# Kernel tuning notes

Hardware: AMD Instinct MI355X
Metric: run time of the kernel (lower is better)

Reference implementation:

```python
import jax, jax.numpy as jnp
import numpy as np

D_MODEL = 1024
N_HEADS = 16
D_HEAD = 64
GROUP_SIZE = 2
N_GROUPS = N_HEADS // GROUP_SIZE


def setup_inputs() -> dict:
    key = jax.random.key(0)
    k1, k2, k3, k4, k5 = jax.random.split(key, 5)
    def xavier(k, shape):
        fan_in, fan_out = shape[0], int(np.prod(shape[1:]))
        bound = float(np.sqrt(6.0 / (fan_in + fan_out)))
        return jax.random.uniform(k, shape, jnp.float32, -bound, bound)
    return {
        'resid': jax.random.normal(k1, (2, 2048, D_MODEL), jnp.float32),
        'W_Q': xavier(k2, (D_MODEL, N_HEADS, D_HEAD)),
        'W_K': xavier(k3, (D_MODEL, N_GROUPS, D_HEAD)),
        'W_V': xavier(k4, (D_MODEL, N_GROUPS, D_HEAD)),
        'W_out': xavier(k5, (D_HEAD, N_HEADS, D_MODEL)),
        'b_out': jnp.zeros((D_MODEL,), jnp.float32),
    }


def reference(resid, W_Q, W_K, W_V, W_out, b_out):
    batch, seq, _ = resid.shape
    # q: [b, s, n_heads, d_head] -> [b, s, n_groups, group_size, d_head]
    q = jnp.einsum('bsd,dhe->bshe', resid, W_Q)
    q = q.reshape(batch, seq, N_GROUPS, GROUP_SIZE, D_HEAD)
    k = jnp.einsum('bsd,dge->bsge', resid, W_K)  # [b, s, g, e]
    v = jnp.einsum('bsd,dge->bsge', resid, W_V)
    # scores: [b, g, group_size, qseq, kseq]
    scores = jnp.einsum('bqgre,bkge->bgrqk', q, k) / jnp.sqrt(jnp.float32(D_HEAD))
    causal_mask = jnp.triu(jnp.ones((seq, seq), bool), k=1)
    scores = jnp.where(causal_mask, jnp.float32(-1000000.0), scores)
    probs = jax.nn.softmax(scores, axis=-1)
    # z: [b, q, g, r, e]
    z = jnp.einsum('bgrqk,bkge->bqgre', probs, v)
    z = z.reshape(batch, seq, N_HEADS, D_HEAD)
    out = jnp.einsum('bshe,ehd->bsd', z, W_out) + b_out
    return out
```

## Files before the change

### kernel.cpp

```cpp
#include <hip/hip_runtime.h>

#define BATCH   2
#define SEQ     2048
#define DMODEL  1024
#define NHEADS  16
#define DHEAD   64
#define NGROUPS 8
#define NTOK    (BATCH * SEQ)
#define QKV_N   2048

typedef unsigned short ushort_t;
typedef unsigned int u32;
typedef __attribute__((ext_vector_type(8))) short short8;
typedef __attribute__((ext_vector_type(4))) float f32x4;

#define MFMA16(a, b, c) __builtin_amdgcn_mfma_f32_16x16x32_bf16((a), (b), (c), 0, 0, 0)

#define GLOAD16(gp, lp)                                                        \
    __builtin_amdgcn_global_load_lds(                                          \
        (const u32 __attribute__((address_space(1)))*)(gp),                    \
        (u32 __attribute__((address_space(3)))*)(lp), 16, 0, 0)

__device__ __forceinline__ ushort_t f2bu(float x) {
    unsigned u = __builtin_bit_cast(unsigned, x);
    unsigned r = (u + 0x7fffu + ((u >> 16) & 1u)) >> 16;
    return (ushort_t)r;
}

__global__ __launch_bounds__(256) void cvt_resid(
    const float* __restrict__ in, ushort_t* __restrict__ out)
{
    const int i4 = blockIdx.x * 256 + threadIdx.x;
    union { float4 v; float f[4]; } a;
    a.v = *reinterpret_cast<const float4*>(in + (size_t)i4 * 4);
    union { uint2 v; ushort_t u[4]; } o;
    #pragma unroll
    for (int j = 0; j < 4; ++j) o.u[j] = f2bu(a.f[j]);
    *reinterpret_cast<uint2*>(out + (size_t)i4 * 4) = o.v;
}

__global__ __launch_bounds__(256) void tr_wqkv(
    const float* __restrict__ Wq, const float* __restrict__ Wk,
    const float* __restrict__ Wv, ushort_t* __restrict__ Wt)
{
    __shared__ float Ws[64][65];
    const int t  = threadIdx.x;
    const int k0 = blockIdx.x * 64;
    const int n0 = blockIdx.y * 64;

    const float* src; int stride, boff;
    if (n0 < 1024)       { src = Wq; stride = 1024; boff = n0; }
    else if (n0 < 1536)  { src = Wk; stride = 512;  boff = n0 - 1024; }
    else                 { src = Wv; stride = 512;  boff = n0 - 1536; }

    #pragma unroll
    for (int i = 0; i < 4; ++i) {
        const int c = i * 256 + t;
        const int row = c >> 4, cc = (c & 15) * 4;
        union { float4 v; float f[4]; } a;
        a.v = *reinterpret_cast<const float4*>(src + (size_t)(k0 + row) * stride + boff + cc);
        #pragma unroll
        for (int j = 0; j < 4; ++j) Ws[row][cc + j] = a.f[j];
    }
    __syncthreads();
    #pragma unroll
    for (int i = 0; i < 2; ++i) {
        const int c = i * 256 + t;
        const int nr = c >> 3, kc = (c & 7) * 8;
        union { uint4 v; ushort_t u[8]; } o;
        #pragma unroll
        for (int j = 0; j < 8; ++j) o.u[j] = f2bu(Ws[kc + j][nr]);
        *reinterpret_cast<uint4*>(Wt + (size_t)(n0 + nr) * 1024 + k0 + kc) = o.v;
    }
}

__global__ __launch_bounds__(256) void tr_wout(
    const float* __restrict__ Wout, ushort_t* __restrict__ Wt)
{
    __shared__ float Ws[64][65];
    const int t  = threadIdx.x;
    const int d0 = blockIdx.x * 64;
    const int h  = blockIdx.y;

    #pragma unroll
    for (int i = 0; i < 4; ++i) {
        const int c = i * 256 + t;
        const int e = c >> 4, dd = (c & 15) * 4;
        union { float4 v; float f[4]; } a;
        a.v = *reinterpret_cast<const float4*>(Wout + (size_t)(e * 16 + h) * 1024 + d0 + dd);
        #pragma unroll
        for (int j = 0; j < 4; ++j) Ws[e][dd + j] = a.f[j];
    }
    __syncthreads();
    #pragma unroll
    for (int i = 0; i < 2; ++i) {
        const int c = i * 256 + t;
        const int dr = c >> 3, ec = (c & 7) * 8;
        union { uint4 v; ushort_t u[8]; } o;
        #pragma unroll
        for (int j = 0; j < 8; ++j) o.u[j] = f2bu(Ws[ec + j][dr]);
        *reinterpret_cast<uint4*>(Wt + (size_t)(d0 + dr) * 1024 + h * 64 + ec) = o.v;
    }
}

__global__ __launch_bounds__(256) void tr_v(
    const ushort_t* __restrict__ qkv, ushort_t* __restrict__ Vt)
{
    __shared__ ushort_t T[64][72];
    const int t  = threadIdx.x;
    const int s0 = blockIdx.x * 64;
    const int g  = blockIdx.y;
    const int b  = blockIdx.z;

    #pragma unroll
    for (int i = 0; i < 2; ++i) {
        const int c = i * 256 + t;
        const int row = c >> 3, ec = (c & 7) * 8;
        *reinterpret_cast<uint4*>(&T[row][ec]) =
            *reinterpret_cast<const uint4*>(
                qkv + (size_t)(b * SEQ + s0 + row) * QKV_N + 1536 + g * 64 + ec);
    }
    __syncthreads();
    #pragma unroll
    for (int i = 0; i < 2; ++i) {
        const int c = i * 256 + t;
        const int er = c >> 3, sc = (c & 7) * 8;
        union { uint4 v; ushort_t u[8]; } o;
        #pragma unroll
        for (int j = 0; j < 8; ++j) o.u[j] = T[sc + j][er];
        *reinterpret_cast<uint4*>(
            Vt + (size_t)((b * NGROUPS + g) * 64 + er) * SEQ + s0 + sc) = o.v;
    }
}

__global__ __launch_bounds__(256) void qkv_gemm(
    const ushort_t* __restrict__ A, const ushort_t* __restrict__ Bt,
    ushort_t* __restrict__ C)
{
    __shared__ ushort_t As[128][32];
    __shared__ ushort_t Bs[128][32];

    const int t = threadIdx.x;
    const int wave = t >> 6, lane = t & 63;
    const int quad = lane >> 4, x = lane & 15;
    const int wm = (wave >> 1) * 64, wn = (wave & 1) * 64;
    const int m0 = blockIdx.y * 128, n0 = blockIdx.x * 128;

    const int sr = lane >> 2;
    const int gc = (lane & 3) ^ (sr & 3);

    f32x4 acc[4][4];
    #pragma unroll
    for (int i = 0; i < 4; ++i)
        #pragma unroll
        for (int j = 0; j < 4; ++j) acc[i][j] = (f32x4)(0.f);

    const int swz = (quad ^ (x & 3)) * 8;

    for (int k0 = 0; k0 < 1024; k0 += 32) {
        #pragma unroll
        for (int s = 0; s < 2; ++s) {
            const int r0 = (wave * 2 + s) * 16;
            GLOAD16(A  + (size_t)(m0 + r0 + sr) * 1024 + k0 + gc * 8, &As[r0][0]);
            GLOAD16(Bt + (size_t)(n0 + r0 + sr) * 1024 + k0 + gc * 8, &Bs[r0][0]);
        }
        __syncthreads();
        short8 af[4], bf[4];
        #pragma unroll
        for (int mt = 0; mt < 4; ++mt)
            af[mt] = *reinterpret_cast<const short8*>(&As[wm + mt * 16 + x][swz]);
        #pragma unroll
        for (int nt = 0; nt < 4; ++nt)
            bf[nt] = *reinterpret_cast<const short8*>(&Bs[wn + nt * 16 + x][swz]);
        #pragma unroll
        for (int mt = 0; mt < 4; ++mt)
            #pragma unroll
            for (int nt = 0; nt < 4; ++nt)
                acc[mt][nt] = MFMA16(af[mt], bf[nt], acc[mt][nt]);
        __syncthreads();
    }

    #pragma unroll
    for (int mt = 0; mt < 4; ++mt)
        #pragma unroll
        for (int nt = 0; nt < 4; ++nt)
            #pragma unroll
            for (int r = 0; r < 4; ++r) {
                const int row = m0 + wm + mt * 16 + quad * 4 + r;
                const int col = n0 + wn + nt * 16 + x;
                C[(size_t)row * QKV_N + col] = f2bu(acc[mt][nt][r]);
            }
}

__global__ __launch_bounds__(256) void out_gemm(
    const ushort_t* __restrict__ A, const ushort_t* __restrict__ Bt,
    const float* __restrict__ bias, float* __restrict__ C)
{
    __shared__ ushort_t As[128][32];
    __shared__ ushort_t Bs[64][32];

    const int t = threadIdx.x;
    const int wave = t >> 6, lane = t & 63;
    const int quad = lane >> 4, x = lane & 15;
    const int wm = (wave >> 1) * 64, wn = (wave & 1) * 32;
    const int m0 = blockIdx.y * 128, n0 = blockIdx.x * 64;

    const int sr = lane >> 2;
    const int gc = (lane & 3) ^ (sr & 3);

    f32x4 acc[4][2];
    #pragma unroll
    for (int i = 0; i < 4; ++i)
        #pragma unroll
        for (int j = 0; j < 2; ++j) acc[i][j] = (f32x4)(0.f);

    const int swz = (quad ^ (x & 3)) * 8;

    for (int k0 = 0; k0 < 1024; k0 += 32) {
        #pragma unroll
        for (int s = 0; s < 2; ++s) {
            const int r0 = (wave * 2 + s) * 16;
            GLOAD16(A + (size_t)(m0 + r0 + sr) * 1024 + k0 + gc * 8, &As[r0][0]);
        }
        {
            const int r0 = wave * 16;
            GLOAD16(Bt + (size_t)(n0 + r0 + sr) * 1024 + k0 + gc * 8, &Bs[r0][0]);
        }
        __syncthreads();
        short8 af[4], bf[2];
        #pragma unroll
        for (int mt = 0; mt < 4; ++mt)
            af[mt] = *reinterpret_cast<const short8*>(&As[wm + mt * 16 + x][swz]);
        #pragma unroll
        for (int nt = 0; nt < 2; ++nt)
            bf[nt] = *reinterpret_cast<const short8*>(&Bs[wn + nt * 16 + x][swz]);
        #pragma unroll
        for (int mt = 0; mt < 4; ++mt)
            #pragma unroll
            for (int nt = 0; nt < 2; ++nt)
                acc[mt][nt] = MFMA16(af[mt], bf[nt], acc[mt][nt]);
        __syncthreads();
    }

    float bv[2];
    #pragma unroll
    for (int nt = 0; nt < 2; ++nt) bv[nt] = bias[n0 + wn + nt * 16 + x];

    #pragma unroll
    for (int mt = 0; mt < 4; ++mt)
        #pragma unroll
        for (int nt = 0; nt < 2; ++nt)
            #pragma unroll
            for (int r = 0; r < 4; ++r) {
                const int row = m0 + wm + mt * 16 + quad * 4 + r;
                const int col = n0 + wn + nt * 16 + x;
                C[(size_t)row * 1024 + col] = acc[mt][nt][r] + bv[nt];
            }
}

__global__ __launch_bounds__(512, 4) void attn(
    const ushort_t* __restrict__ qkv, const ushort_t* __restrict__ Vt,
    ushort_t* __restrict__ z)
{
    __shared__ ushort_t smem[3 * 64 * 72];
    ushort_t (*Ks)[72]  = (ushort_t(*)[72])(smem);
    ushort_t (*Vts)[72] = (ushort_t(*)[72])(smem + 64 * 72);
    ushort_t (*Ps)[72]  = (ushort_t(*)[72])(smem + 2 * 64 * 72);
    float* Ob = (float*)smem;
    float* Lb = (float*)(smem + 2 * 64 * 72);

    const int t = threadIdx.x;
    const int wave = t >> 6, lane = t & 63;
    const int quad = lane >> 4, x = lane & 15;
    const int rw = wave & 3;
    const int kw = wave >> 2;

    const int h  = blockIdx.x;
    const int qp = blockIdx.y;
    const int b  = blockIdx.z;
    const int g  = h >> 1;

    const int srow = t >> 3;
    const int sec  = (t & 7) * 8;

    const ushort_t* kbase = qkv + (size_t)(b * SEQ) * QKV_N + 1024 + g * DHEAD + sec;
    const ushort_t* vbase = Vt + (size_t)((b * NGROUPS + g) * 64 + srow) * SEQ + sec;

    #pragma unroll
    for (int phase = 0; phase < 2; ++phase) {
        const int qt = phase ? (31 - qp) : qp;
        const int qrow0 = qt * 64;

        short8 aq[2];
        {
            const size_t qr = (size_t)(b * SEQ + qrow0 + rw * 16 + x);
            #pragma unroll
            for (int ks = 0; ks < 2; ++ks)
                aq[ks] = *reinterpret_cast<const short8*>(
                    qkv + qr * QKV_N + h * DHEAD + ks * 32 + quad * 8);
        }

        f32x4 o[4];
        #pragma unroll
        for (int nt = 0; nt < 4; ++nt) o[nt] = (f32x4)(0.f);
        float l_acc[4] = {0.f, 0.f, 0.f, 0.f};

        uint4 kr, vr;
        kr = *reinterpret_cast<const uint4*>(kbase + (size_t)srow * QKV_N);
        vr = *reinterpret_cast<const uint4*>(vbase);

        for (int kt = 0; kt <= qt; ++kt) {
            __syncthreads();
            *reinterpret_cast<uint4*>(&Ks[srow][sec])  = kr;
            *reinterpret_cast<uint4*>(&Vts[srow][sec]) = vr;
            __syncthreads();

            if (kt < qt) {
                kr = *reinterpret_cast<const uint4*>(
                    kbase + (size_t)((kt + 1) * 64 + srow) * QKV_N);
                vr = *reinterpret_cast<const uint4*>(vbase + (kt + 1) * 64);
            }

            const bool diag  = (kt == qt);
            const bool wlive = !diag || (kw * 32 <= rw * 16 + 15);

            if (wlive) {
                f32x4 s[2];
                __builtin_amdgcn_s_setprio(1);
                #pragma unroll
                for (int nt = 0; nt < 2; ++nt) {
                    const bool live = !diag || (kw * 32 + nt * 16 <= rw * 16 + 15);
                    if (live) {
                        s[nt] = (f32x4)(0.f);
                        #pragma unroll
                        for (int ks = 0; ks < 2; ++ks) {
                            short8 bk = *reinterpret_cast<const short8*>(
                                &Ks[kw * 32 + nt * 16 + x][ks * 32 + quad * 8]);
                            s[nt] = MFMA16(aq[ks], bk, s[nt]);
                        }
                    }
                }
                __builtin_amdgcn_s_setprio(0);

                #pragma unroll
                for (int r = 0; r < 4; ++r) {
                    #pragma unroll
                    for (int nt = 0; nt < 2; ++nt) {
                        const bool live = !diag || (kw * 32 + nt * 16 <= rw * 16 + 15);
                        float p = 0.f;
                        if (live) {
                            const bool masked = diag &&
                                (kw * 32 + nt * 16 + x > rw * 16 + quad * 4 + r);
                            p = masked ? 0.f : __expf(s[nt][r] * 0.125f);
                        }
                        l_acc[r] += p;
                        Ps[rw * 16 + quad * 4 + r][kw * 32 + nt * 16 + x] = f2bu(p);
                    }
                }

                __builtin_amdgcn_s_setprio(1);
                {
                    short8 ap = *reinterpret_cast<const short8*>(
                        &Ps[rw * 16 + x][kw * 32 + quad * 8]);
                    #pragma unroll
                    for (int nt = 0; nt < 4; ++nt) {
                        short8 bv = *reinterpret_cast<const short8*>(
                            &Vts[nt * 16 + x][kw * 32 + quad * 8]);
                        o[nt] = MFMA16(ap, bv, o[nt]);
                    }
                }
                __builtin_amdgcn_s_setprio(0);
            }
        }

        __syncthreads();
        if (kw == 1) {
            #pragma unroll
            for (int nt = 0; nt < 4; ++nt)
                #pragma unroll
                for (int r = 0; r < 4; ++r)
                    Ob[(rw * 16 + quad * 4 + r) * 64 + nt * 16 + x] = o[nt][r];
            #pragma unroll
            for (int r = 0; r < 4; ++r)
                Lb[(rw * 16 + quad * 4 + r) * 16 + x] = l_acc[r];
        }
        __syncthreads();
        if (kw == 0) {
            #pragma unroll
            for (int nt = 0; nt < 4; ++nt)
                #pragma unroll
                for (int r = 0; r < 4; ++r)
                    o[nt][r] += Ob[(rw * 16 + quad * 4 + r) * 64 + nt * 16 + x];
            float inv[4];
            #pragma unroll
            for (int r = 0; r < 4; ++r) {
                float lr = l_acc[r] + Lb[(rw * 16 + quad * 4 + r) * 16 + x];
                #pragma unroll
                for (int off = 1; off < 16; off <<= 1)
                    lr += __shfl_xor(lr, off);
                inv[r] = 1.f / lr;
            }
            #pragma unroll
            for (int nt = 0; nt < 4; ++nt)
                #pragma unroll
                for (int r = 0; r < 4; ++r) {
                    const int row = qrow0 + rw * 16 + quad * 4 + r;
                    z[(size_t)(b * SEQ + row) * 1024 + h * DHEAD + nt * 16 + x] =
                        f2bu(o[nt][r] * inv[r]);
                }
        }
    }
}

extern "C" void kernel_launch(void* const* d_in, const int* in_sizes, int n_in,
                              void* d_out, int out_size, void* d_ws, size_t ws_size,
                              hipStream_t stream)
{
    const float* resid = (const float*)d_in[0];
    const float* Wq    = (const float*)d_in[1];
    const float* Wk    = (const float*)d_in[2];
    const float* Wv    = (const float*)d_in[3];
    const float* Wout  = (const float*)d_in[4];
    const float* bout  = (const float*)d_in[5];
    float* out = (float*)d_out;

    ushort_t* rbf   = (ushort_t*)d_ws;
    ushort_t* wqkvt = rbf   + (size_t)NTOK * DMODEL;
    ushort_t* woutt = wqkvt + (size_t)QKV_N * DMODEL;
    ushort_t* qkv   = woutt + (size_t)DMODEL * DMODEL;
    ushort_t* z     = qkv   + (size_t)NTOK * QKV_N;
    ushort_t* vt    = rbf;

    cvt_resid<<<dim3(NTOK * DMODEL / 1024), 256, 0, stream>>>(resid, rbf);
    tr_wqkv  <<<dim3(16, 32), 256, 0, stream>>>(Wq, Wk, Wv, wqkvt);
    tr_wout  <<<dim3(16, 16), 256, 0, stream>>>(Wout, woutt);
    qkv_gemm <<<dim3(16, 32), 256, 0, stream>>>(rbf, wqkvt, qkv);
    tr_v     <<<dim3(SEQ / 64, NGROUPS, BATCH), 256, 0, stream>>>(qkv, vt);
    attn     <<<dim3(16, 16, 2), 512, 0, stream>>>(qkv, vt, z);
    out_gemm <<<dim3(16, 32), 256, 0, stream>>>(z, woutt, bout, out);
}
```

Measured before the change: 179.9 us.

## Fuse prep kernels, deepen GEMM K-tiles, swizzle attention LDS, MFMA row sums

Merges the three conversion/transpose kernels into one launch dispatched by block index, removing two kernel launches. Both GEMMs now stage 64-wide K tiles with an XOR swizzle over 8 chunks, halving the number of barrier-separated iterations at the cost of doubled LDS footprint. The attention kernel drops row padding in favour of XOR-swizzled K, V and P tiles, and computes softmax row sums with an extra MFMA against a ones vector instead of scalar accumulation plus a shuffle reduction. This adds one MFMA per step and depends on the swizzle indices matching between writes and reads.

```diff
diff --git a/kernel.cpp b/kernel.cpp
--- a/kernel.cpp
+++ b/kernel.cpp
@@ -27,79 +27,86 @@
     return (ushort_t)r;
 }
 
-__global__ __launch_bounds__(256) void cvt_resid(
-    const float* __restrict__ in, ushort_t* __restrict__ out)
-{
-    const int i4 = blockIdx.x * 256 + threadIdx.x;
-    union { float4 v; float f[4]; } a;
-    a.v = *reinterpret_cast<const float4*>(in + (size_t)i4 * 4);
-    union { uint2 v; ushort_t u[4]; } o;
-    #pragma unroll
-    for (int j = 0; j < 4; ++j) o.u[j] = f2bu(a.f[j]);
-    *reinterpret_cast<uint2*>(out + (size_t)i4 * 4) = o.v;
-}
-
-__global__ __launch_bounds__(256) void tr_wqkv(
+__global__ __launch_bounds__(256) void prep(
+    const float* __restrict__ resid,
     const float* __restrict__ Wq, const float* __restrict__ Wk,
-    const float* __restrict__ Wv, ushort_t* __restrict__ Wt)
+    const float* __restrict__ Wv, const float* __restrict__ Wout,
+    ushort_t* __restrict__ rbf, ushort_t* __restrict__ Wt,
+    ushort_t* __restrict__ Wot)
 {
     __shared__ float Ws[64][65];
-    const int t  = threadIdx.x;
-    const int k0 = blockIdx.x * 64;
-    const int n0 = blockIdx.y * 64;
-
-    const float* src; int stride, boff;
-    if (n0 < 1024)       { src = Wq; stride = 1024; boff = n0; }
-    else if (n0 < 1536)  { src = Wk; stride = 512;  boff = n0 - 1024; }
-    else                 { src = Wv; stride = 512;  boff = n0 - 1536; }
-
-    #pragma unroll
-    for (int i = 0; i < 4; ++i) {
-        const int c = i * 256 + t;
-        const int row = c >> 4, cc = (c & 15) * 4;
+    const int t = threadIdx.x;
+    const int bid = blockIdx.x;
+
+    if (bid < 4096) {
+        const int i4 = bid * 256 + t;
         union { float4 v; float f[4]; } a;
-        a.v = *reinterpret_cast<const float4*>(src + (size_t)(k0 + row) * stride + boff + cc);
-        #pragma unroll
-        for (int j = 0; j < 4; ++j) Ws[row][cc + j] = a.f[j];
-    }
-    __syncthreads();
-    #pragma unroll
-    for (int i = 0; i < 2; ++i) {
-        const int c = i * 256 + t;
-        const int nr = c >> 3, kc = (c & 7) * 8;
-        union { uint4 v; ushort_t u[8]; } o;
-        #pragma unroll
-        for (int j = 0; j < 8; ++j) o.u[j] = f2bu(Ws[kc + j][nr]);
-        *reinterpret_cast<uint4*>(Wt + (size_t)(n0 + nr) * 1024 + k0 + kc) = o.v;
-    }
-}
-
-__global__ __launch_bounds__(256) void tr_wout(
-    const float* __restrict__ Wout, ushort_t* __restrict__ Wt)
-{
-    __shared__ float Ws[64][65];
-    const int t  = threadIdx.x;
-    const int d0 = blockIdx.x * 64;
-    const int h  = blockIdx.y;
-
-    #pragma unroll
-    for (int i = 0; i < 4; ++i) {
-        const int c = i * 256 + t;
-        const int e = c >> 4, dd = (c & 15) * 4;
-        union { float4 v; float f[4]; } a;
-        a.v = *reinterpret_cast<const float4*>(Wout + (size_t)(e * 16 + h) * 1024 + d0 + dd);
-        #pragma unroll
-        for (int j = 0; j < 4; ++j) Ws[e][dd + j] = a.f[j];
-    }
-    __syncthreads();
-    #pragma unroll
-    for (int i = 0; i < 2; ++i) {
-        const int c = i * 256 + t;
-        const int dr = c >> 3, ec = (c & 7) * 8;
-        union { uint4 v; ushort_t u[8]; } o;
-        #pragma unroll
-        for (int j = 0; j < 8; ++j) o.u[j] = f2bu(Ws[ec + j][dr]);
-        *reinterpret_cast<uint4*>(Wt + (size_t)(d0 + dr) * 1024 + h * 64 + ec) = o.v;
+        a.v = *reinterpret_cast<const float4*>(resid + (size_t)i4 * 4);
+        union { uint2 v; ushort_t u[4]; } o;
+        #pragma unroll
+        for (int j = 0; j < 4; ++j) o.u[j] = f2bu(a.f[j]);
+        *reinterpret_cast<uint2*>(rbf + (size_t)i4 * 4) = o.v;
+        return;
+    }
+
+    if (bid < 4096 + 512) {
+        const int rel = bid - 4096;
+        const int k0 = (rel & 15) * 64;
+        const int n0 = (rel >> 4) * 64;
+
+        const float* src; int stride, boff;
+        if (n0 < 1024)       { src = Wq; stride = 1024; boff = n0; }
+        else if (n0 < 1536)  { src = Wk; stride = 512;  boff = n0 - 1024; }
+        else                 { src = Wv; stride = 512;  boff = n0 - 1536; }
+
+        #pragma unroll
+        for (int i = 0; i < 4; ++i) {
+            const int c = i * 256 + t;
+            const int row = c >> 4, cc = (c & 15) * 4;
+            union { float4 v; float f[4]; } a;
+            a.v = *reinterpret_cast<const float4*>(
+                src + (size_t)(k0 + row) * stride + boff + cc);
+            #pragma unroll
+            for (int j = 0; j < 4; ++j) Ws[row][cc + j] = a.f[j];
+        }
+        __syncthreads();
+        #pragma unroll
+        for (int i = 0; i < 2; ++i) {
+            const int c = i * 256 + t;
+            const int nr = c >> 3, kc = (c & 7) * 8;
+            union { uint4 v; ushort_t u[8]; } o;
+            #pragma unroll
+            for (int j = 0; j < 8; ++j) o.u[j] = f2bu(Ws[kc + j][nr]);
+            *reinterpret_cast<uint4*>(Wt + (size_t)(n0 + nr) * 1024 + k0 + kc) = o.v;
+        }
+        return;
+    }
+
+    {
+        const int rel = bid - 4608;
+        const int d0 = (rel & 15) * 64;
+        const int h  = rel >> 4;
+
+        #pragma unroll
+        for (int i = 0; i < 4; ++i) {
+            const int c = i * 256 + t;
+            const int e = c >> 4, dd = (c & 15) * 4;
+            union { float4 v; float f[4]; } a;
+            a.v = *reinterpret_cast<const float4*>(
+                Wout + (size_t)(e * 16 + h) * 1024 + d0 + dd);
+            #pragma unroll
+            for (int j = 0; j < 4; ++j) Ws[e][dd + j] = a.f[j];
+        }
+        __syncthreads();
+        #pragma unroll
+        for (int i = 0; i < 2; ++i) {
+            const int c = i * 256 + t;
+            const int dr = c >> 3, ec = (c & 7) * 8;
+            union { uint4 v; ushort_t u[8]; } o;
+            #pragma unroll
+            for (int j = 0; j < 8; ++j) o.u[j] = f2bu(Ws[ec + j][dr]);
+            *reinterpret_cast<uint4*>(Wot + (size_t)(d0 + dr) * 1024 + h * 64 + ec) = o.v;
+        }
     }
 }
 
@@ -137,8 +144,8 @@
     const ushort_t* __restrict__ A, const ushort_t* __restrict__ Bt,
     ushort_t* __restrict__ C)
 {
-    __shared__ ushort_t As[128][32];
-    __shared__ ushort_t Bs[128][32];
+    __shared__ ushort_t As[128][64];
+    __shared__ ushort_t Bs[128][64];
 
     const int t = threadIdx.x;
     const int wave = t >> 6, lane = t & 63;
@@ -146,8 +153,8 @@
     const int wm = (wave >> 1) * 64, wn = (wave & 1) * 64;
     const int m0 = blockIdx.y * 128, n0 = blockIdx.x * 128;
 
-    const int sr = lane >> 2;
-    const int gc = (lane & 3) ^ (sr & 3);
+    const int sr8 = lane >> 3;
+    const int gc  = (lane & 7) ^ sr8;
 
     f32x4 acc[4][4];
     #pragma unroll
@@ -155,28 +162,30 @@
         #pragma unroll
         for (int j = 0; j < 4; ++j) acc[i][j] = (f32x4)(0.f);
 
-    const int swz = (quad ^ (x & 3)) * 8;
-
-    for (int k0 = 0; k0 < 1024; k0 += 32) {
-        #pragma unroll
-        for (int s = 0; s < 2; ++s) {
-            const int r0 = (wave * 2 + s) * 16;
-            GLOAD16(A  + (size_t)(m0 + r0 + sr) * 1024 + k0 + gc * 8, &As[r0][0]);
-            GLOAD16(Bt + (size_t)(n0 + r0 + sr) * 1024 + k0 + gc * 8, &Bs[r0][0]);
-        }
-        __syncthreads();
-        short8 af[4], bf[4];
-        #pragma unroll
-        for (int mt = 0; mt < 4; ++mt)
-            af[mt] = *reinterpret_cast<const short8*>(&As[wm + mt * 16 + x][swz]);
-        #pragma unroll
-        for (int nt = 0; nt < 4; ++nt)
-            bf[nt] = *reinterpret_cast<const short8*>(&Bs[wn + nt * 16 + x][swz]);
-        #pragma unroll
-        for (int mt = 0; mt < 4; ++mt)
+    for (int k0 = 0; k0 < 1024; k0 += 64) {
+        #pragma unroll
+        for (int s = 0; s < 4; ++s) {
+            const int r0 = (wave * 4 + s) * 8;
+            GLOAD16(A  + (size_t)(m0 + r0 + sr8) * 1024 + k0 + gc * 8, &As[r0][0]);
+            GLOAD16(Bt + (size_t)(n0 + r0 + sr8) * 1024 + k0 + gc * 8, &Bs[r0][0]);
+        }
+        __syncthreads();
+        #pragma unroll
+        for (int j = 0; j < 2; ++j) {
+            const int cs = ((j * 4 + quad) ^ (x & 7)) * 8;
+            short8 af[4], bf[4];
+            #pragma unroll
+            for (int mt = 0; mt < 4; ++mt)
+                af[mt] = *reinterpret_cast<const short8*>(&As[wm + mt * 16 + x][cs]);
             #pragma unroll
             for (int nt = 0; nt < 4; ++nt)
-                acc[mt][nt] = MFMA16(af[mt], bf[nt], acc[mt][nt]);
+                bf[nt] = *reinterpret_cast<const short8*>(&Bs[wn + nt * 16 + x][cs]);
+            #pragma unroll
+            for (int mt = 0; mt < 4; ++mt)
+                #pragma unroll
+                for (int nt = 0; nt < 4; ++nt)
+                    acc[mt][nt] = MFMA16(af[mt], bf[nt], acc[mt][nt]);
+        }
         __syncthreads();
     }
 
@@ -196,8 +205,8 @@
     const ushort_t* __restrict__ A, const ushort_t* __restrict__ Bt,
     const float* __restrict__ bias, float* __restrict__ C)
 {
-    __shared__ ushort_t As[128][32];
-    __shared__ ushort_t Bs[64][32];
+    __shared__ ushort_t As[128][64];
+    __shared__ ushort_t Bs[64][64];
 
     const int t = threadIdx.x;
     const int wave = t >> 6, lane = t & 63;
@@ -205,8 +214,8 @@
     const int wm = (wave >> 1) * 64, wn = (wave & 1) * 32;
     const int m0 = blockIdx.y * 128, n0 = blockIdx.x * 64;
 
-    const int sr = lane >> 2;
-    const int gc = (lane & 3) ^ (sr & 3);
+    const int sr8 = lane >> 3;
+    const int gc  = (lane & 7) ^ sr8;
 
     f32x4 acc[4][2];
     #pragma unroll
@@ -214,31 +223,34 @@
         #pragma unroll
         for (int j = 0; j < 2; ++j) acc[i][j] = (f32x4)(0.f);
 
-    const int swz = (quad ^ (x & 3)) * 8;
-
-    for (int k0 = 0; k0 < 1024; k0 += 32) {
+    for (int k0 = 0; k0 < 1024; k0 += 64) {
+        #pragma unroll
+        for (int s = 0; s < 4; ++s) {
+            const int r0 = (wave * 4 + s) * 8;
+            GLOAD16(A + (size_t)(m0 + r0 + sr8) * 1024 + k0 + gc * 8, &As[r0][0]);
+        }
         #pragma unroll
         for (int s = 0; s < 2; ++s) {
-            const int r0 = (wave * 2 + s) * 16;
-            GLOAD16(A + (size_t)(m0 + r0 + sr) * 1024 + k0 + gc * 8, &As[r0][0]);
-        }
-        {
-            const int r0 = wave * 16;
-            GLOAD16(Bt + (size_t)(n0 + r0 + sr) * 1024 + k0 + gc * 8, &Bs[r0][0]);
-        }
-        __syncthreads();
-        short8 af[4], bf[2];
-        #pragma unroll
-        for (int mt = 0; mt < 4; ++mt)
-            af[mt] = *reinterpret_cast<const short8*>(&As[wm + mt * 16 + x][swz]);
-        #pragma unroll
-        for (int nt = 0; nt < 2; ++nt)
-            bf[nt] = *reinterpret_cast<const short8*>(&Bs[wn + nt * 16 + x][swz]);
-        #pragma unroll
-        for (int mt = 0; mt < 4; ++mt)
+            const int r0 = (wave * 2 + s) * 8;
+            GLOAD16(Bt + (size_t)(n0 + r0 + sr8) * 1024 + k0 + gc * 8, &Bs[r0][0]);
+        }
+        __syncthreads();
+        #pragma unroll
+        for (int j = 0; j < 2; ++j) {
+            const int cs = ((j * 4 + quad) ^ (x & 7)) * 8;
+            short8 af[4], bf[2];
+            #pragma unroll
+            for (int mt = 0; mt < 4; ++mt)
+                af[mt] = *reinterpret_cast<const short8*>(&As[wm + mt * 16 + x][cs]);
             #pragma unroll
             for (int nt = 0; nt < 2; ++nt)
-                acc[mt][nt] = MFMA16(af[mt], bf[nt], acc[mt][nt]);
+                bf[nt] = *reinterpret_cast<const short8*>(&Bs[wn + nt * 16 + x][cs]);
+            #pragma unroll
+            for (int mt = 0; mt < 4; ++mt)
+                #pragma unroll
+                for (int nt = 0; nt < 2; ++nt)
+                    acc[mt][nt] = MFMA16(af[mt], bf[nt], acc[mt][nt]);
+        }
         __syncthreads();
     }
 
@@ -262,12 +274,12 @@
     const ushort_t* __restrict__ qkv, const ushort_t* __restrict__ Vt,
     ushort_t* __restrict__ z)
 {
-    __shared__ ushort_t smem[3 * 64 * 72];
-    ushort_t (*Ks)[72]  = (ushort_t(*)[72])(smem);
-    ushort_t (*Vts)[72] = (ushort_t(*)[72])(smem + 64 * 72);
-    ushort_t (*Ps)[72]  = (ushort_t(*)[72])(smem + 2 * 64 * 72);
+    __shared__ ushort_t smem[3 * 64 * 64];
+    ushort_t (*Ks)[64]  = (ushort_t(*)[64])(smem);
+    ushort_t (*Vts)[64] = (ushort_t(*)[64])(smem + 64 * 64);
+    ushort_t (*Ps)[64]  = (ushort_t(*)[64])(smem + 2 * 64 * 64);
     float* Ob = (float*)smem;
-    float* Lb = (float*)(smem + 2 * 64 * 72);
+    float* Lb = (float*)(smem + 2 * 64 * 64);
 
     const int t = threadIdx.x;
     const int wave = t >> 6, lane = t & 63;
@@ -281,10 +293,15 @@
     const int g  = h >> 1;
 
     const int srow = t >> 3;
+    const int schk = (t & 7) ^ (srow & 7);
     const int sec  = (t & 7) * 8;
 
     const ushort_t* kbase = qkv + (size_t)(b * SEQ) * QKV_N + 1024 + g * DHEAD + sec;
     const ushort_t* vbase = Vt + (size_t)((b * NGROUPS + g) * 64 + srow) * SEQ + sec;
+
+    short8 ones;
+    #pragma unroll
+    for (int i = 0; i < 8; ++i) ones[i] = (short)0x3F80;
 
     #pragma unroll
     for (int phase = 0; phase < 2; ++phase) {
@@ -303,7 +320,7 @@
         f32x4 o[4];
         #pragma unroll
         for (int nt = 0; nt < 4; ++nt) o[nt] = (f32x4)(0.f);
-        float l_acc[4] = {0.f, 0.f, 0.f, 0.f};
+        f32x4 lacc = (f32x4)(0.f);
 
         uint4 kr, vr;
         kr = *reinterpret_cast<const uint4*>(kbase + (size_t)srow * QKV_N);
@@ -311,8 +328,8 @@
 
         for (int kt = 0; kt <= qt; ++kt) {
             __syncthreads();
-            *reinterpret_cast<uint4*>(&Ks[srow][sec])  = kr;
-            *reinterpret_cast<uint4*>(&Vts[srow][sec]) = vr;
+            *reinterpret_cast<uint4*>(&Ks[srow][schk * 8])  = kr;
+            *reinterpret_cast<uint4*>(&Vts[srow][schk * 8]) = vr;
             __syncthreads();
 
             if (kt < qt) {
@@ -334,8 +351,9 @@
                         s[nt] = (f32x4)(0.f);
                         #pragma unroll
                         for (int ks = 0; ks < 2; ++ks) {
+                            const int cs = ((ks * 4 + quad) ^ (x & 7)) * 8;
                             short8 bk = *reinterpret_cast<const short8*>(
-                                &Ks[kw * 32 + nt * 16 + x][ks * 32 + quad * 8]);
+                                &Ks[kw * 32 + nt * 16 + x][cs]);
                             s[nt] = MFMA16(aq[ks], bk, s[nt]);
                         }
                     }
@@ -344,6 +362,8 @@
 
                 #pragma unroll
                 for (int r = 0; r < 4; ++r) {
+                    const int prow = rw * 16 + quad * 4 + r;
+                    const int pswz = (prow & 7) << 3;
                     #pragma unroll
                     for (int nt = 0; nt < 2; ++nt) {
                         const bool live = !diag || (kw * 32 + nt * 16 <= rw * 16 + 15);
@@ -353,21 +373,22 @@
                                 (kw * 32 + nt * 16 + x > rw * 16 + quad * 4 + r);
                             p = masked ? 0.f : __expf(s[nt][r] * 0.125f);
                         }
-                        l_acc[r] += p;
-                        Ps[rw * 16 + quad * 4 + r][kw * 32 + nt * 16 + x] = f2bu(p);
+                        Ps[prow][(kw * 32 + nt * 16 + x) ^ pswz] = f2bu(p);
                     }
                 }
 
                 __builtin_amdgcn_s_setprio(1);
                 {
+                    const int cap = ((kw * 4 + quad) ^ (x & 7)) * 8;
                     short8 ap = *reinterpret_cast<const short8*>(
-                        &Ps[rw * 16 + x][kw * 32 + quad * 8]);
+                        &Ps[rw * 16 + x][cap]);
                     #pragma unroll
                     for (int nt = 0; nt < 4; ++nt) {
                         short8 bv = *reinterpret_cast<const short8*>(
-                            &Vts[nt * 16 + x][kw * 32 + quad * 8]);
+                            &Vts[nt * 16 + x][cap]);
                         o[nt] = MFMA16(ap, bv, o[nt]);
                     }
+                    lacc = MFMA16(ap, ones, lacc);
                 }
                 __builtin_amdgcn_s_setprio(0);
             }
@@ -382,7 +403,7 @@
                     Ob[(rw * 16 + quad * 4 + r) * 64 + nt * 16 + x] = o[nt][r];
             #pragma unroll
             for (int r = 0; r < 4; ++r)
-                Lb[(rw * 16 + quad * 4 + r) * 16 + x] = l_acc[r];
+                Lb[(rw * 16 + quad * 4 + r) * 16 + x] = lacc[r];
         }
         __syncthreads();
         if (kw == 0) {
@@ -393,13 +414,8 @@
                     o[nt][r] += Ob[(rw * 16 + quad * 4 + r) * 64 + nt * 16 + x];
             float inv[4];
             #pragma unroll
-            for (int r = 0; r < 4; ++r) {
-                float lr = l_acc[r] + Lb[(rw * 16 + quad * 4 + r) * 16 + x];
-                #pragma unroll
-                for (int off = 1; off < 16; off <<= 1)
-                    lr += __shfl_xor(lr, off);
-                inv[r] = 1.f / lr;
-            }
+            for (int r = 0; r < 4; ++r)
+                inv[r] = 1.f / (lacc[r] + Lb[(rw * 16 + quad * 4 + r) * 16 + x]);
             #pragma unroll
             for (int nt = 0; nt < 4; ++nt)
                 #pragma unroll
@@ -431,9 +447,8 @@
     ushort_t* z     = qkv   + (size_t)NTOK * QKV_N;
     ushort_t* vt    = rbf;
 
-    cvt_resid<<<dim3(NTOK * DMODEL / 1024), 256, 0, stream>>>(resid, rbf);
-    tr_wqkv  <<<dim3(16, 32), 256, 0, stream>>>(Wq, Wk, Wv, wqkvt);
-    tr_wout  <<<dim3(16, 16), 256, 0, stream>>>(Wout, woutt);
+    prep     <<<dim3(4864), 256, 0, stream>>>(resid, Wq, Wk, Wv, Wout,
+                                              rbf, wqkvt, woutt);
     qkv_gemm <<<dim3(16, 32), 256, 0, stream>>>(rbf, wqkvt, qkv);
     tr_v     <<<dim3(SEQ / 64, NGROUPS, BATCH), 256, 0, stream>>>(qkv, vt);
     attn     <<<dim3(16, 16, 2), 512, 0, stream>>>(qkv, vt, z);
```

New measurement: 164.6 us. -8.5%, faster.
